# Kernel optimization log

Hardware: AMD Instinct MI355X
Metric: run time of the kernel (lower is better)

## Reference

```python
import jax, jax.numpy as jnp
import numpy as np


def setup_inputs() -> dict:
    key = jax.random.key(0)
    k1, k2, k3 = jax.random.split(key, 3)
    B, R, N, A, U = 64, 5, 512, 64, 128
    adjacency = jax.random.uniform(k1, (B, R, N, N), dtype=jnp.float32)
    features = jax.random.normal(k2, (B, N, A), dtype=jnp.float32)
    kernel = jax.random.normal(k3, (R, A, U), dtype=jnp.float32) * 0.05
    bias = jnp.zeros((R, 1, U), dtype=jnp.float32)
    return {"adjacency": adjacency, "features": features, "kernel": kernel, "bias": bias}


def reference(adjacency, features, kernel, bias):
    # adjacency: [B, R, N, N], features: [B, N, A]
    # aggregate neighbourhoods per relation: [B, R, N, A]
    agg = jnp.einsum("brnm,bma->brna", adjacency, features)
    # relation-wise projection: [B, R, N, U]
    dp = jnp.einsum("brna,rau->brnu", agg, kernel) + bias  # bias broadcasts over B, N
    # sum over relation axis, then activation: [B, N, U]
    return jax.nn.relu(jnp.sum(dp, axis=1))
```

## Files before the change

kernel.cpp:

```cpp
#include <hip/hip_runtime.h>
#include <hip/hip_bf16.h>

typedef __attribute__((ext_vector_type(4))) float f32x4;
typedef __attribute__((ext_vector_type(8))) short s16x8;
typedef __attribute__((ext_vector_type(4))) short s16x4;

__device__ __forceinline__ unsigned short f2bf(float f) {
  __hip_bfloat16 h = __float2bfloat16(f);
  return __builtin_bit_cast(unsigned short, h);
}

__global__ void k_ft(const float* __restrict__ F, unsigned short* __restrict__ FT) {
  __shared__ float t[64][65];
  const int b  = blockIdx.x >> 3;
  const int m0 = (blockIdx.x & 7) * 64;
  const int tid = threadIdx.x;
  {
    const int row = tid >> 2, ac = (tid & 3) * 16;
    const float* src = F + ((size_t)b * 512 + m0 + row) * 64 + ac;
    #pragma unroll
    for (int j = 0; j < 4; ++j) {
      f32x4 v = *(const f32x4*)(src + j * 4);
      t[row][ac + j * 4 + 0] = v[0]; t[row][ac + j * 4 + 1] = v[1];
      t[row][ac + j * 4 + 2] = v[2]; t[row][ac + j * 4 + 3] = v[3];
    }
  }
  __syncthreads();
  {
    const int a = tid >> 2, mc = (tid & 3) * 16;
    unsigned short* dst = FT + ((size_t)b * 64 + a) * 512 + m0 + mc;
    s16x8 p0, p1;
    #pragma unroll
    for (int j = 0; j < 8; ++j) {
      p0[j] = (short)f2bf(t[mc + j][a]);
      p1[j] = (short)f2bf(t[mc + 8 + j][a]);
    }
    *(s16x8*)(dst) = p0;
    *(s16x8*)(dst + 8) = p1;
  }
}

__global__ void k_kt(const float* __restrict__ K, const float* __restrict__ bias,
                     unsigned short* __restrict__ KT, float* __restrict__ bsum) {
  const int gtid = threadIdx.x + blockIdx.x * blockDim.x;
  for (int idx = gtid; idx < 128 * 320; idx += blockDim.x * gridDim.x) {
    const int u = idx / 320, ra = idx % 320;
    KT[idx] = f2bf(K[(size_t)ra * 128 + u]);
  }
  if (gtid < 128) {
    float s = 0.f;
    #pragma unroll
    for (int r = 0; r < 5; ++r) s += bias[r * 128 + gtid];
    bsum[gtid] = s;
  }
}

__global__ __launch_bounds__(256, 2) void k_fused(const float* __restrict__ Adj,
                                                  const unsigned short* __restrict__ FT,
                                                  const unsigned short* __restrict__ KT,
                                                  const float* __restrict__ bsum,
                                                  float* __restrict__ out) {
  __shared__ unsigned short q[4][2][16][136];
  __shared__ unsigned short ag[4][16][328];
  const int b  = blockIdx.x >> 3;
  const int nt = blockIdx.x & 7;
  const int w  = threadIdx.x >> 6;
  const int l  = threadIdx.x & 63;
  const int l15 = l & 15, g = l >> 4;

  const float* adjW = Adj + (size_t)b * 5 * 262144 + (size_t)(nt * 64 + w * 16) * 512;
  const unsigned short* ftW = FT + (size_t)b * 64 * 512;
  const int srow = l >> 5;
  const int scol = (l & 31) * 4;

  unsigned short (*Q)[16][136] = q[w];
  unsigned short (*agw)[328] = ag[w];

  f32x4 G[8];
  #pragma unroll
  for (int i = 0; i < 8; ++i)
    G[i] = *(const f32x4*)(adjW + (size_t)(i * 2 + srow) * 512 + scol);
  #pragma unroll
  for (int i = 0; i < 8; ++i) {
    s16x4 pk;
    pk[0] = (short)f2bf(G[i][0]); pk[1] = (short)f2bf(G[i][1]);
    pk[2] = (short)f2bf(G[i][2]); pk[3] = (short)f2bf(G[i][3]);
    *(s16x4*)&Q[0][i * 2 + srow][scol] = pk;
  }

  f32x4 acc[5][4];
  #pragma unroll
  for (int r = 0; r < 5; ++r)
    #pragma unroll
    for (int at = 0; at < 4; ++at) acc[r][at] = (f32x4)0.f;

  int cur = 0;
  for (int ks4 = 0; ks4 < 4; ++ks4) {
    s16x8 ffrag[4][4];
    #pragma unroll
    for (int ksl = 0; ksl < 4; ++ksl)
      #pragma unroll
      for (int at = 0; at < 4; ++at)
        ffrag[ksl][at] = *(const s16x8*)(ftW + (size_t)(at * 16 + l15) * 512 + ks4 * 128 + ksl * 32 + g * 8);

    #pragma unroll
    for (int r = 0; r < 5; ++r) {
      const bool have_next = (r < 4) || (ks4 < 3);
      if (have_next) {
        const int rn = (r == 4) ? 0 : r + 1;
        const int kn = (r == 4) ? ks4 + 1 : ks4;
        const float* p = adjW + (size_t)rn * 262144 + (size_t)kn * 128;
        #pragma unroll
        for (int i = 0; i < 8; ++i)
          G[i] = *(const f32x4*)(p + (size_t)(i * 2 + srow) * 512 + scol);
      }

      #pragma unroll
      for (int ksl = 0; ksl < 4; ++ksl) {
        s16x8 bfrag = *(const s16x8*)&Q[cur][l15][ksl * 32 + g * 8];
        acc[r][0] = __builtin_amdgcn_mfma_f32_16x16x32_bf16(ffrag[ksl][0], bfrag, acc[r][0], 0, 0, 0);
        acc[r][1] = __builtin_amdgcn_mfma_f32_16x16x32_bf16(ffrag[ksl][1], bfrag, acc[r][1], 0, 0, 0);
        acc[r][2] = __builtin_amdgcn_mfma_f32_16x16x32_bf16(ffrag[ksl][2], bfrag, acc[r][2], 0, 0, 0);
        acc[r][3] = __builtin_amdgcn_mfma_f32_16x16x32_bf16(ffrag[ksl][3], bfrag, acc[r][3], 0, 0, 0);
      }

      if (have_next) {
        #pragma unroll
        for (int i = 0; i < 8; ++i) {
          s16x4 pk;
          pk[0] = (short)f2bf(G[i][0]); pk[1] = (short)f2bf(G[i][1]);
          pk[2] = (short)f2bf(G[i][2]); pk[3] = (short)f2bf(G[i][3]);
          *(s16x4*)&Q[cur ^ 1][i * 2 + srow][scol] = pk;
        }
        cur ^= 1;
      }
    }
  }

  #pragma unroll
  for (int r = 0; r < 5; ++r)
    #pragma unroll
    for (int at = 0; at < 4; ++at) {
      s16x4 pk;
      pk[0] = (short)f2bf(acc[r][at][0]); pk[1] = (short)f2bf(acc[r][at][1]);
      pk[2] = (short)f2bf(acc[r][at][2]); pk[3] = (short)f2bf(acc[r][at][3]);
      *(s16x4*)&agw[l15][r * 64 + at * 16 + g * 4] = pk;
    }

  f32x4 o[8];
  #pragma unroll
  for (int ut = 0; ut < 8; ++ut) o[ut] = (f32x4)0.f;

  #pragma unroll 2
  for (int ks = 0; ks < 10; ++ks) {
    s16x8 af = *(const s16x8*)&agw[l15][ks * 32 + g * 8];
    #pragma unroll
    for (int ut = 0; ut < 8; ++ut) {
      s16x8 kf = *(const s16x8*)(KT + (size_t)(ut * 16 + l15) * 320 + ks * 32 + g * 8);
      o[ut] = __builtin_amdgcn_mfma_f32_16x16x32_bf16(af, kf, o[ut], 0, 0, 0);
    }
  }

  #pragma unroll
  for (int ut = 0; ut < 8; ++ut) {
    const int u = ut * 16 + l15;
    const float bs = bsum[u];
    float* op = out + ((size_t)b * 512 + nt * 64 + w * 16 + g * 4) * 128 + u;
    #pragma unroll
    for (int t = 0; t < 4; ++t) {
      float vv = o[ut][t] + bs;
      op[(size_t)t * 128] = vv > 0.f ? vv : 0.f;
    }
  }
}

extern "C" void kernel_launch(void* const* d_in, const int* in_sizes, int n_in,
                              void* d_out, int out_size, void* d_ws, size_t ws_size,
                              hipStream_t stream) {
  const float* adj  = (const float*)d_in[0];
  const float* feat = (const float*)d_in[1];
  const float* kern = (const float*)d_in[2];
  const float* bias = (const float*)d_in[3];
  float* out = (float*)d_out;

  char* ws = (char*)d_ws;
  unsigned short* FT   = (unsigned short*)ws;
  unsigned short* KT   = (unsigned short*)(ws + 4194304);
  float*          bsum = (float*)(ws + 4194304 + 81920);

  hipLaunchKernelGGL(k_ft,    dim3(512), dim3(256), 0, stream, feat, FT);
  hipLaunchKernelGGL(k_kt,    dim3(160), dim3(256), 0, stream, kern, bias, KT, bsum);
  hipLaunchKernelGGL(k_fused, dim3(512), dim3(256), 0, stream, adj, FT, KT, bsum, out);
  (void)in_sizes; (void)n_in; (void)out_size; (void)ws_size;
}
```

Baseline: 97.42 us.

## Stream adjacency tiles directly into LDS via global_load_lds with XOR swizzle

Replaces the register-staged adjacency prefetch (global load to VGPRs, convert to bf16, store to LDS) with direct global-to-LDS async copies of fp32 data, using an XOR-swizzled layout and explicit vmcnt waits for double buffering. The bf16 conversion now happens after reading from LDS, right before the MFMA. The aggregation scratch buffer reuses the same LDS region, which shrinks shared memory use. The aim is to free VGPRs and issue slots and overlap loads better. The cost is twice the LDS footprint per tile and twice the LDS read traffic, and correctness now depends on manual wait counts and the swizzle being consistent.

```diff
diff --git a/kernel.cpp b/kernel.cpp
--- a/kernel.cpp
+++ b/kernel.cpp
@@ -9,6 +9,9 @@
   __hip_bfloat16 h = __float2bfloat16(f);
   return __builtin_bit_cast(unsigned short, h);
 }
+
+#define AS1U(p) ((const __attribute__((address_space(1))) unsigned int*)(p))
+#define AS3U(p) ((__attribute__((address_space(3))) unsigned int*)(p))
 
 __global__ void k_ft(const float* __restrict__ F, unsigned short* __restrict__ FT) {
   __shared__ float t[64][65];
@@ -60,8 +63,7 @@
                                                   const unsigned short* __restrict__ KT,
                                                   const float* __restrict__ bsum,
                                                   float* __restrict__ out) {
-  __shared__ unsigned short q[4][2][16][136];
-  __shared__ unsigned short ag[4][16][328];
+  __shared__ __align__(16) float shq[4][2][16][128];
   const int b  = blockIdx.x >> 3;
   const int nt = blockIdx.x & 7;
   const int w  = threadIdx.x >> 6;
@@ -71,21 +73,15 @@
   const float* adjW = Adj + (size_t)b * 5 * 262144 + (size_t)(nt * 64 + w * 16) * 512;
   const unsigned short* ftW = FT + (size_t)b * 64 * 512;
   const int srow = l >> 5;
-  const int scol = (l & 31) * 4;
-
-  unsigned short (*Q)[16][136] = q[w];
-  unsigned short (*agw)[328] = ag[w];
-
-  f32x4 G[8];
-  #pragma unroll
-  for (int i = 0; i < 8; ++i)
-    G[i] = *(const f32x4*)(adjW + (size_t)(i * 2 + srow) * 512 + scol);
+  const int c16  = (l & 31) * 16;
+
+  float* qw = &shq[w][0][0][0];
+
   #pragma unroll
   for (int i = 0; i < 8; ++i) {
-    s16x4 pk;
-    pk[0] = (short)f2bf(G[i][0]); pk[1] = (short)f2bf(G[i][1]);
-    pk[2] = (short)f2bf(G[i][2]); pk[3] = (short)f2bf(G[i][3]);
-    *(s16x4*)&Q[0][i * 2 + srow][scol] = pk;
+    const int xr = (2 * i) & 7;
+    const float* src = adjW + (size_t)(2 * i + srow) * 512 + ((c16 ^ ((xr + srow) << 4)) >> 2);
+    __builtin_amdgcn_global_load_lds(AS1U(src), AS3U(qw + i * 256), 16, 0, 0);
   }
 
   f32x4 acc[5][4];
@@ -94,7 +90,7 @@
     #pragma unroll
     for (int at = 0; at < 4; ++at) acc[r][at] = (f32x4)0.f;
 
-  int cur = 0;
+  #pragma unroll
   for (int ks4 = 0; ks4 < 4; ++ks4) {
     s16x8 ffrag[4][4];
     #pragma unroll
@@ -105,38 +101,47 @@
 
     #pragma unroll
     for (int r = 0; r < 5; ++r) {
-      const bool have_next = (r < 4) || (ks4 < 3);
+      const int s = ks4 * 5 + r;
+      const int cur = s & 1;
+      const bool have_next = (s < 19);
       if (have_next) {
         const int rn = (r == 4) ? 0 : r + 1;
         const int kn = (r == 4) ? ks4 + 1 : ks4;
-        const float* p = adjW + (size_t)rn * 262144 + (size_t)kn * 128;
+        const float* sb = adjW + (size_t)rn * 262144 + kn * 128;
         #pragma unroll
-        for (int i = 0; i < 8; ++i)
-          G[i] = *(const f32x4*)(p + (size_t)(i * 2 + srow) * 512 + scol);
+        for (int i = 0; i < 8; ++i) {
+          const int xr = (2 * i) & 7;
+          const float* src = sb + (size_t)(2 * i + srow) * 512 + ((c16 ^ ((xr + srow) << 4)) >> 2);
+          __builtin_amdgcn_global_load_lds(AS1U(src), AS3U(qw + (cur ^ 1) * 2048 + i * 256), 16, 0, 0);
+        }
+        asm volatile("s_waitcnt vmcnt(8)" ::: "memory");
+      } else {
+        asm volatile("s_waitcnt vmcnt(0)" ::: "memory");
       }
-
+      __builtin_amdgcn_sched_barrier(0);
+
+      const char* qr = (const char*)(qw + cur * 2048 + l15 * 128);
+      const int x = (l15 & 7) << 4;
       #pragma unroll
       for (int ksl = 0; ksl < 4; ++ksl) {
-        s16x8 bfrag = *(const s16x8*)&Q[cur][l15][ksl * 32 + g * 8];
+        const int C = ksl * 128 + g * 32;
+        f32x4 lo = *(const f32x4*)(qr + (C ^ x));
+        f32x4 hi = *(const f32x4*)(qr + ((C + 16) ^ x));
+        s16x8 bfrag;
+        #pragma unroll
+        for (int j = 0; j < 4; ++j) {
+          bfrag[j]     = (short)f2bf(lo[j]);
+          bfrag[4 + j] = (short)f2bf(hi[j]);
+        }
         acc[r][0] = __builtin_amdgcn_mfma_f32_16x16x32_bf16(ffrag[ksl][0], bfrag, acc[r][0], 0, 0, 0);
         acc[r][1] = __builtin_amdgcn_mfma_f32_16x16x32_bf16(ffrag[ksl][1], bfrag, acc[r][1], 0, 0, 0);
         acc[r][2] = __builtin_amdgcn_mfma_f32_16x16x32_bf16(ffrag[ksl][2], bfrag, acc[r][2], 0, 0, 0);
         acc[r][3] = __builtin_amdgcn_mfma_f32_16x16x32_bf16(ffrag[ksl][3], bfrag, acc[r][3], 0, 0, 0);
       }
-
-      if (have_next) {
-        #pragma unroll
-        for (int i = 0; i < 8; ++i) {
-          s16x4 pk;
-          pk[0] = (short)f2bf(G[i][0]); pk[1] = (short)f2bf(G[i][1]);
-          pk[2] = (short)f2bf(G[i][2]); pk[3] = (short)f2bf(G[i][3]);
-          *(s16x4*)&Q[cur ^ 1][i * 2 + srow][scol] = pk;
-        }
-        cur ^= 1;
-      }
-    }
-  }
-
+    }
+  }
+
+  unsigned short* agw = (unsigned short*)qw;
   #pragma unroll
   for (int r = 0; r < 5; ++r)
     #pragma unroll
@@ -144,7 +149,7 @@
       s16x4 pk;
       pk[0] = (short)f2bf(acc[r][at][0]); pk[1] = (short)f2bf(acc[r][at][1]);
       pk[2] = (short)f2bf(acc[r][at][2]); pk[3] = (short)f2bf(acc[r][at][3]);
-      *(s16x4*)&agw[l15][r * 64 + at * 16 + g * 4] = pk;
+      *(s16x4*)&agw[l15 * 328 + r * 64 + at * 16 + g * 4] = pk;
     }
 
   f32x4 o[8];
@@ -153,7 +158,7 @@
 
   #pragma unroll 2
   for (int ks = 0; ks < 10; ++ks) {
-    s16x8 af = *(const s16x8*)&agw[l15][ks * 32 + g * 8];
+    s16x8 af = *(const s16x8*)&agw[l15 * 328 + ks * 32 + g * 8];
     #pragma unroll
     for (int ut = 0; ut < 8; ++ut) {
       s16x8 kf = *(const s16x8*)(KT + (size_t)(ut * 16 + l15) * 320 + ks * 32 + g * 8);
```

New measurement: 92.76 us. -4.8%, faster.
